# Kernel tuning notes

Hardware: AMD Instinct MI355X
Metric: run time of the kernel (lower is better)

## Reference

```python
import jax, jax.numpy as jnp
import numpy as np

B, L, H, K = 64, 2048, 256, 32  # batch, padded seq len, hidden dim, n event types


def setup_inputs() -> dict:
    key = jax.random.key(0)
    ks = jax.random.split(key, 11)
    event_seqs = jax.random.randint(ks[0], (B, L), 0, K)
    # ragged lengths; original code requires 1 <= seq_len <= L-1
    seqs_length = jax.random.randint(ks[1], (B,), 1, L - 1)
    total_time_seqs = jax.random.uniform(ks[2], (B,), minval=10.0, maxval=100.0)
    hidden_t = jax.random.normal(ks[3], (L, B, H))
    cell_t = jax.random.normal(ks[4], (L, B, H))
    cell_target_t = jax.random.normal(ks[5], (L, B, H))
    output_t = jax.random.uniform(ks[6], (L, B, H))          # output gate in (0,1)
    decay_t = jax.random.uniform(ks[7], (L, B, H))           # positive decay rates
    # mimics original bug: uniform(0, total_time_seqs[0]) for every row, shape [L, B]
    sim_time_seqs = jax.random.uniform(ks[8], (L, B), maxval=total_time_seqs[0])
    W_int = jax.random.normal(ks[9], (H, K)) * (1.0 / np.sqrt(H))
    b_int = jax.random.normal(ks[10], (K,)) * 0.01
    return dict(event_seqs=event_seqs, seqs_length=seqs_length,
                total_time_seqs=total_time_seqs, hidden_t=hidden_t,
                cell_t=cell_t, cell_target_t=cell_target_t, output_t=output_t,
                decay_t=decay_t, sim_time_seqs=sim_time_seqs, W_int=W_int, b_int=b_int)


def reference(event_seqs, seqs_length, total_time_seqs, hidden_t, cell_t,
              cell_target_t, output_t, decay_t, sim_time_seqs, W_int, b_int):
    # intensity_layer: softplus(Linear(H -> K)); log-intensity [L, B, K]
    log_intensity = jnp.log(jax.nn.softplus(
        jnp.einsum('lbh,hk->lbk', hidden_t, W_int) + b_int))

    # ragged mask over time steps: valid t < seq_len, shape [B, L]
    mask = jnp.arange(L)[None, :] < seqs_length[:, None]

    # term 1: sum_b sum_{t<len_b} log_intensity[t, b, event_seqs[b, t+1]]
    # shift events left by one; last column is always masked (seq_len <= L-1)
    shifted = jnp.concatenate([event_seqs[:, 1:], event_seqs[:, :1]], axis=1)  # [B, L]
    li_b = jnp.transpose(log_intensity, (1, 0, 2))                              # [B, L, K]
    gathered = jnp.take_along_axis(li_b, shifted[:, :, None], axis=2)[..., 0]   # [B, L]
    original_ll = jnp.sum(jnp.where(mask, gathered, 0.0))

    # term 2: Monte Carlo integral of intensity at simulated durations
    # decay_cell: c(t) = c_target + (c - c_target) * exp(-decay * dt); h = o * tanh(c)
    c_sim = cell_target_t + (cell_t - cell_target_t) * jnp.exp(
        -decay_t * sim_time_seqs[:, :, None])                                   # [L, B, H]
    h_sim = output_t * jnp.tanh(c_sim)
    sim_intensity = jax.nn.softplus(
        jnp.einsum('lbh,hk->lbk', h_sim, W_int) + b_int)                        # [L, B, K]
    per_b = jnp.sum(jnp.where(mask, sim_intensity.sum(-1).T, 0.0), axis=1)      # [B]
    mc_coef = total_time_seqs / seqs_length.astype(total_time_seqs.dtype)
    simulated_ll = jnp.sum(mc_coef * per_b)

    return -(original_ll - simulated_ll)
```

## Files before the change

### kernel.cpp

```cpp
#include <hip/hip_runtime.h>

#define LL 2048
#define BB 64
#define HH 256
#define KK 32

#define NB  768
#define WPB 4

typedef __attribute__((ext_vector_type(8))) short  short8;
typedef __attribute__((ext_vector_type(4))) float  f32x4;

__device__ __forceinline__ float softplus_f(float x) {
    return x > 20.f ? x : __logf(1.f + __expf(x));
}
__device__ __forceinline__ unsigned f2bf(float x) {
    unsigned u = __builtin_bit_cast(unsigned, x);
    return (u + 0x7FFFu + ((u >> 16) & 1u)) >> 16;
}

struct RowT { float4 h, c, t, o, d; };

__global__ __launch_bounds__(256, 3) void nhll_main(
    const int*   __restrict__ events,
    const int*   __restrict__ lens,
    const float* __restrict__ ttime,
    const float* __restrict__ hidden,
    const float* __restrict__ cell,
    const float* __restrict__ ctarg,
    const float* __restrict__ outp,
    const float* __restrict__ decay,
    const float* __restrict__ simt,
    const float* __restrict__ W,
    const float* __restrict__ bias,
    float*       __restrict__ partial)
{
    __shared__ __align__(16) char  WTs[KK * HH * 2];
    __shared__ __align__(16) char  Als[WPB][16 * HH * 2];
    __shared__ int   pfx[BB + 1];
    __shared__ float coef_s[BB];
    __shared__ float wacc[WPB];

    const int tid  = threadIdx.x;
    const int lane = tid & 63;
    const int q    = tid >> 6;
    const int g    = lane >> 4;
    const int m    = lane & 15;

    {
        const float* wrow = &W[tid * KK];
#pragma unroll
        for (int k = 0; k < KK; ++k) {
            const int byte = (k * 512 + tid * 2) ^ ((k & 7) << 4);
            *(unsigned short*)(WTs + byte) = (unsigned short)f2bf(wrow[k]);
        }
    }
    if (tid < BB) {
        const int ln = lens[tid];
        coef_s[tid] = ttime[tid] / (float)ln;
        int s = ln;
#pragma unroll
        for (int mm = 1; mm < 64; mm <<= 1) {
            const int t = __shfl_up(s, mm, 64);
            if (lane >= mm) s += t;
        }
        pfx[tid + 1] = s;
        if (tid == 0) pfx[0] = 0;
    }
    __syncthreads();

    const float b_lo = bias[m];
    const float b_hi = bias[16 + m];
    const int   T      = pfx[BB];
    const int   ntiles = (T + 7) >> 3;
    char* Aw = Als[q];
    float acc = 0.f;

    for (int tile = blockIdx.x * WPB + q; tile < ntiles; tile += NB * WPB) {
        int i = tile * 8 + (lane & 7);
        const int valid = (i < T) ? 1 : 0;
        if (!valid) i = T - 1;
        int lo = 0, hi = BB;
#pragma unroll
        for (int s = 0; s < 6; ++s) {
            const int mid = (lo + hi) >> 1;
            if (pfx[mid] <= i) lo = mid; else hi = mid;
        }
        const int   b    = lo;
        const int   l    = i - pfx[b];
        const int   r    = l * BB + b;
        const float st   = simt[r];
        const float coef = valid ? coef_s[b] : 0.f;
        const int   e    = events[b * LL + l + 1];

        int   rs[8]; float ss[8];
#pragma unroll
        for (int j = 0; j < 8; ++j) {
            rs[j] = __shfl(r, j, 64);
            ss[j] = __shfl(st, j, 64);
        }

        auto LD = [&](int rr_) -> RowT {
            const int base = rr_ * HH + lane * 4;
            RowT x;
            x.h = *(const float4*)(hidden + base);
            x.c = *(const float4*)(cell   + base);
            x.t = *(const float4*)(ctarg  + base);
            x.o = *(const float4*)(outp   + base);
            x.d = *(const float4*)(decay  + base);
            return x;
        };
        auto ST = [&](int j, const RowT& R, float stv) {
            float4 v;
            float cs, e2;
            cs = R.t.x + (R.c.x - R.t.x) * __expf(-R.d.x * stv); e2 = __expf(2.f * cs); v.x = R.o.x * ((e2 - 1.f) / (e2 + 1.f));
            cs = R.t.y + (R.c.y - R.t.y) * __expf(-R.d.y * stv); e2 = __expf(2.f * cs); v.y = R.o.y * ((e2 - 1.f) / (e2 + 1.f));
            cs = R.t.z + (R.c.z - R.t.z) * __expf(-R.d.z * stv); e2 = __expf(2.f * cs); v.z = R.o.z * ((e2 - 1.f) / (e2 + 1.f));
            cs = R.t.w + (R.c.w - R.t.w) * __expf(-R.d.w * stv); e2 = __expf(2.f * cs); v.w = R.o.w * ((e2 - 1.f) / (e2 + 1.f));
            const int swz = (j & 7) << 4;
            *(uint2*)(Aw + ((j * 512 + lane * 8) ^ swz)) =
                make_uint2(f2bf(v.x) | (f2bf(v.y) << 16), f2bf(v.z) | (f2bf(v.w) << 16));
            *(uint2*)(Aw + (((8 + j) * 512 + lane * 8) ^ swz)) =
                make_uint2(f2bf(R.h.x) | (f2bf(R.h.y) << 16), f2bf(R.h.z) | (f2bf(R.h.w) << 16));
        };

        RowT buf[3];
        buf[0] = LD(rs[0]); buf[1] = LD(rs[1]); buf[2] = LD(rs[2]);
#pragma unroll
        for (int j = 0; j < 8; ++j) {
            ST(j, buf[j % 3], ss[j]);
            if (j + 3 < 8) buf[j % 3] = LD(rs[j + 3]);
        }

        f32x4 C0 = {0.f,0.f,0.f,0.f}, C1 = {0.f,0.f,0.f,0.f};
        const int abase = m * 512 + 16 * g;
        const int swz   = (m & 7) << 4;
#pragma unroll
        for (int c = 0; c < 8; ++c) {
            const short8 a  = *(const short8*)(Aw  + ((abase + 64 * c) ^ swz));
            const short8 w0 = *(const short8*)(WTs + ((abase + 64 * c) ^ swz));
            const short8 w1 = *(const short8*)(WTs + ((abase + 8192 + 64 * c) ^ swz));
            C0 = __builtin_amdgcn_mfma_f32_16x16x32_bf16(a, w0, C0, 0, 0, 0);
            C1 = __builtin_amdgcn_mfma_f32_16x16x32_bf16(a, w1, C1, 0, 0, 0);
        }

        float sp[4];
#pragma unroll
        for (int reg = 0; reg < 4; ++reg)
            sp[reg] = softplus_f(C0[reg] + b_lo) + softplus_f(C1[reg] + b_hi);
#pragma unroll
        for (int mk = 1; mk <= 8; mk <<= 1) {
#pragma unroll
            for (int reg = 0; reg < 4; ++reg) sp[reg] += __shfl_xor(sp[reg], mk, 64);
        }
        float t2 = 0.f;
#pragma unroll
        for (int reg = 0; reg < 4; ++reg) {
            const float cf = __shfl(coef, 4 * g + reg, 64);
            t2 += cf * sp[reg];
        }
        if (m == 0 && g < 2) acc += t2;

        float kv = 0.f, kb = 0.f;
#pragma unroll
        for (int rr = 0; rr < 8; ++rr) {
            const int   er   = __shfl(e, rr, 64);
            const float cand = (er < 16) ? C0[rr & 3] : C1[rr & 3];
            const float val  = __shfl(cand, 32 + ((rr >> 2) << 4) + (er & 15), 64);
            const float bsel = (er < 16) ? b_lo : b_hi;
            const float be   = __shfl(bsel, er & 15, 64);
            if (lane == rr) { kv = val; kb = be; }
        }
        if (lane < 8 && valid)
            acc -= __logf(softplus_f(kv + kb));
    }

#pragma unroll
    for (int mk = 1; mk < 64; mk <<= 1) acc += __shfl_xor(acc, mk, 64);
    if (lane == 0) wacc[q] = acc;
    __syncthreads();
    if (tid == 0) partial[blockIdx.x] = wacc[0] + wacc[1] + wacc[2] + wacc[3];
}

__global__ __launch_bounds__(256) void nhll_finalize(
    const float* __restrict__ partial, float* __restrict__ out)
{
    __shared__ float red[4];
    float s = 0.f;
    for (int i = threadIdx.x; i < NB; i += 256) s += partial[i];
    for (int mk = 1; mk < 64; mk <<= 1) s += __shfl_xor(s, mk, 64);
    if ((threadIdx.x & 63) == 0) red[threadIdx.x >> 6] = s;
    __syncthreads();
    if (threadIdx.x == 0)
        out[0] = red[0] + red[1] + red[2] + red[3];
}

extern "C" void kernel_launch(void* const* d_in, const int* in_sizes, int n_in,
                              void* d_out, int out_size, void* d_ws, size_t ws_size,
                              hipStream_t stream) {
    const int*   events = (const int*)  d_in[0];
    const int*   lens   = (const int*)  d_in[1];
    const float* ttime  = (const float*)d_in[2];
    const float* hidden = (const float*)d_in[3];
    const float* cell   = (const float*)d_in[4];
    const float* ctarg  = (const float*)d_in[5];
    const float* outp   = (const float*)d_in[6];
    const float* decay  = (const float*)d_in[7];
    const float* simt   = (const float*)d_in[8];
    const float* W      = (const float*)d_in[9];
    const float* bias   = (const float*)d_in[10];

    float* part = (float*)d_ws;
    float* out  = (float*)d_out;

    nhll_main<<<NB, 256, 0, stream>>>(events, lens, ttime, hidden, cell, ctarg,
                                      outp, decay, simt, W, bias, part);
    nhll_finalize<<<1, 256, 0, stream>>>(part, out);
}
```

Measured before the change: 68.35 us.

## Compute gathered event logit via per-row dot product instead of MFMA rows

The hidden-state rows are no longer staged in LDS for MFMA. For each row, the logit of the next event is computed directly as a dot product of the fp32 hidden row with the bf16 weight column for that event, followed by a wave-wide shuffle reduction. This halves the per-wave A tile in LDS, and with it the number of blocks is raised and launch bounds are bumped to 4 blocks per CU. The cost is six cross-lane shuffle steps per row, plus MFMA lanes 8-15 reading duplicated A rows, in exchange for less LDS traffic and higher occupancy.

```diff
diff --git a/kernel.cpp b/kernel.cpp
--- a/kernel.cpp
+++ b/kernel.cpp
@@ -5,7 +5,7 @@
 #define HH 256
 #define KK 32
 
-#define NB  768
+#define NB  1024
 #define WPB 4
 
 typedef __attribute__((ext_vector_type(8))) short  short8;
@@ -18,10 +18,16 @@
     unsigned u = __builtin_bit_cast(unsigned, x);
     return (u + 0x7FFFu + ((u >> 16) & 1u)) >> 16;
 }
+__device__ __forceinline__ float bfhi(unsigned u) {
+    return __builtin_bit_cast(float, u & 0xFFFF0000u);
+}
+__device__ __forceinline__ float bflo(unsigned u) {
+    return __builtin_bit_cast(float, u << 16);
+}
 
 struct RowT { float4 h, c, t, o, d; };
 
-__global__ __launch_bounds__(256, 3) void nhll_main(
+__global__ __launch_bounds__(256, 4) void nhll_main(
     const int*   __restrict__ events,
     const int*   __restrict__ lens,
     const float* __restrict__ ttime,
@@ -36,7 +42,7 @@
     float*       __restrict__ partial)
 {
     __shared__ __align__(16) char  WTs[KK * HH * 2];
-    __shared__ __align__(16) char  Als[WPB][16 * HH * 2];
+    __shared__ __align__(16) char  Als[WPB][8 * HH * 2];
     __shared__ int   pfx[BB + 1];
     __shared__ float coef_s[BB];
     __shared__ float wacc[WPB];
@@ -93,7 +99,7 @@
         const float coef = valid ? coef_s[b] : 0.f;
         const int   e    = events[b * LL + l + 1];
 
-        int   rs[8]; float ss[8];
+        int rs[8]; float ss[8];
 #pragma unroll
         for (int j = 0; j < 8; ++j) {
             rs[j] = __shfl(r, j, 64);
@@ -117,11 +123,18 @@
             cs = R.t.y + (R.c.y - R.t.y) * __expf(-R.d.y * stv); e2 = __expf(2.f * cs); v.y = R.o.y * ((e2 - 1.f) / (e2 + 1.f));
             cs = R.t.z + (R.c.z - R.t.z) * __expf(-R.d.z * stv); e2 = __expf(2.f * cs); v.z = R.o.z * ((e2 - 1.f) / (e2 + 1.f));
             cs = R.t.w + (R.c.w - R.t.w) * __expf(-R.d.w * stv); e2 = __expf(2.f * cs); v.w = R.o.w * ((e2 - 1.f) / (e2 + 1.f));
-            const int swz = (j & 7) << 4;
-            *(uint2*)(Aw + ((j * 512 + lane * 8) ^ swz)) =
+            *(uint2*)(Aw + ((j * 512 + lane * 8) ^ ((j & 7) << 4))) =
                 make_uint2(f2bf(v.x) | (f2bf(v.y) << 16), f2bf(v.z) | (f2bf(v.w) << 16));
-            *(uint2*)(Aw + (((8 + j) * 512 + lane * 8) ^ swz)) =
-                make_uint2(f2bf(R.h.x) | (f2bf(R.h.y) << 16), f2bf(R.h.z) | (f2bf(R.h.w) << 16));
+
+            const int ej = __shfl(e, j, 64);
+            const uint2 wc = *(const uint2*)(WTs + ((ej * 512 + lane * 8) ^ ((ej & 7) << 4)));
+            float su = R.h.x * bflo(wc.x) + R.h.y * bfhi(wc.x)
+                     + R.h.z * bflo(wc.y) + R.h.w * bfhi(wc.y);
+#pragma unroll
+            for (int mk = 1; mk < 64; mk <<= 1) su += __shfl_xor(su, mk, 64);
+            const float be = __shfl((ej < 16) ? b_lo : b_hi, ej & 15, 64);
+            if (lane == j && valid)
+                acc -= __logf(softplus_f(su + be));
         };
 
         RowT buf[3];
@@ -133,13 +146,14 @@
         }
 
         f32x4 C0 = {0.f,0.f,0.f,0.f}, C1 = {0.f,0.f,0.f,0.f};
-        const int abase = m * 512 + 16 * g;
-        const int swz   = (m & 7) << 4;
+        const int abase = (m & 7) * 512 + 16 * g;
+        const int wbase = m * 512 + 16 * g;
+        const int swza  = (m & 7) << 4;
 #pragma unroll
         for (int c = 0; c < 8; ++c) {
-            const short8 a  = *(const short8*)(Aw  + ((abase + 64 * c) ^ swz));
-            const short8 w0 = *(const short8*)(WTs + ((abase + 64 * c) ^ swz));
-            const short8 w1 = *(const short8*)(WTs + ((abase + 8192 + 64 * c) ^ swz));
+            const short8 a  = *(const short8*)(Aw  + ((abase + 64 * c) ^ swza));
+            const short8 w0 = *(const short8*)(WTs + ((wbase + 64 * c) ^ swza));
+            const short8 w1 = *(const short8*)(WTs + ((wbase + 8192 + 64 * c) ^ swza));
             C0 = __builtin_amdgcn_mfma_f32_16x16x32_bf16(a, w0, C0, 0, 0, 0);
             C1 = __builtin_amdgcn_mfma_f32_16x16x32_bf16(a, w1, C1, 0, 0, 0);
         }
@@ -160,19 +174,6 @@
             t2 += cf * sp[reg];
         }
         if (m == 0 && g < 2) acc += t2;
-
-        float kv = 0.f, kb = 0.f;
-#pragma unroll
-        for (int rr = 0; rr < 8; ++rr) {
-            const int   er   = __shfl(e, rr, 64);
-            const float cand = (er < 16) ? C0[rr & 3] : C1[rr & 3];
-            const float val  = __shfl(cand, 32 + ((rr >> 2) << 4) + (er & 15), 64);
-            const float bsel = (er < 16) ? b_lo : b_hi;
-            const float be   = __shfl(bsel, er & 15, 64);
-            if (lane == rr) { kv = val; kb = be; }
-        }
-        if (lane < 8 && valid)
-            acc -= __logf(softplus_f(kv + kb));
     }
 
 #pragma unroll
```

Result: slower. 119.4 us (+74.7%).

## Software-pipeline next tile's metadata and first row loads across MFMA epilogue

Applied to the files above, without the earlier changes.

Restructures the per-warp tile loop so the next tile's prefix-sum search, sim-time/event loads and first two row loads are issued before the current tile's MFMA and softplus epilogue. This hides global-load latency across tile iterations and removes the lambda-based ring buffer in favour of explicit rotating registers. Bias is also staged in shared memory so the event-bias lookup becomes a direct LDS read instead of a shuffle. The extra live RowT registers raise register pressure and could hurt occupancy under the 3-blocks launch bound.

```diff
diff --git a/kernel.cpp b/kernel.cpp
--- a/kernel.cpp
+++ b/kernel.cpp
@@ -20,6 +20,37 @@
 }
 
 struct RowT { float4 h, c, t, o, d; };
+
+__device__ __forceinline__ RowT load_row(
+    const float* __restrict__ hidden, const float* __restrict__ cell,
+    const float* __restrict__ ctarg,  const float* __restrict__ outp,
+    const float* __restrict__ decay,  int r, int lane)
+{
+    const int base = r * HH + lane * 4;
+    RowT x;
+    x.h = *(const float4*)(hidden + base);
+    x.c = *(const float4*)(cell   + base);
+    x.t = *(const float4*)(ctarg  + base);
+    x.o = *(const float4*)(outp   + base);
+    x.d = *(const float4*)(decay  + base);
+    return x;
+}
+
+template<int J>
+__device__ __forceinline__ void STrow(char* Aw, const RowT& R, float stv, int lane)
+{
+    float4 v;
+    float cs, e2;
+    cs = R.t.x + (R.c.x - R.t.x) * __expf(-R.d.x * stv); e2 = __expf(2.f * cs); v.x = R.o.x * ((e2 - 1.f) / (e2 + 1.f));
+    cs = R.t.y + (R.c.y - R.t.y) * __expf(-R.d.y * stv); e2 = __expf(2.f * cs); v.y = R.o.y * ((e2 - 1.f) / (e2 + 1.f));
+    cs = R.t.z + (R.c.z - R.t.z) * __expf(-R.d.z * stv); e2 = __expf(2.f * cs); v.z = R.o.z * ((e2 - 1.f) / (e2 + 1.f));
+    cs = R.t.w + (R.c.w - R.t.w) * __expf(-R.d.w * stv); e2 = __expf(2.f * cs); v.w = R.o.w * ((e2 - 1.f) / (e2 + 1.f));
+    const int swz = (J & 7) << 4;
+    *(uint2*)(Aw + ((J * 512 + lane * 8) ^ swz)) =
+        make_uint2(f2bf(v.x) | (f2bf(v.y) << 16), f2bf(v.z) | (f2bf(v.w) << 16));
+    *(uint2*)(Aw + (((8 + J) * 512 + lane * 8) ^ swz)) =
+        make_uint2(f2bf(R.h.x) | (f2bf(R.h.y) << 16), f2bf(R.h.z) | (f2bf(R.h.w) << 16));
+}
 
 __global__ __launch_bounds__(256, 3) void nhll_main(
     const int*   __restrict__ events,
@@ -39,6 +70,7 @@
     __shared__ __align__(16) char  Als[WPB][16 * HH * 2];
     __shared__ int   pfx[BB + 1];
     __shared__ float coef_s[BB];
+    __shared__ float bias_s[KK];
     __shared__ float wacc[WPB];
 
     const int tid  = threadIdx.x;
@@ -55,6 +87,7 @@
             *(unsigned short*)(WTs + byte) = (unsigned short)f2bf(wrow[k]);
         }
     }
+    if (tid < KK) bias_s[tid] = bias[tid];
     if (tid < BB) {
         const int ln = lens[tid];
         coef_s[tid] = ttime[tid] / (float)ln;
@@ -69,111 +102,118 @@
     }
     __syncthreads();
 
-    const float b_lo = bias[m];
-    const float b_hi = bias[16 + m];
+    const float b_lo = bias_s[m];
+    const float b_hi = bias_s[16 + m];
     const int   T      = pfx[BB];
     const int   ntiles = (T + 7) >> 3;
+    const int   stride = NB * WPB;
     char* Aw = Als[q];
     float acc = 0.f;
 
-    for (int tile = blockIdx.x * WPB + q; tile < ntiles; tile += NB * WPB) {
-        int i = tile * 8 + (lane & 7);
-        const int valid = (i < T) ? 1 : 0;
-        if (!valid) i = T - 1;
-        int lo = 0, hi = BB;
-#pragma unroll
-        for (int s = 0; s < 6; ++s) {
-            const int mid = (lo + hi) >> 1;
-            if (pfx[mid] <= i) lo = mid; else hi = mid;
+#define META(TILE, R_, ST_, E_, CF_, V_) do {                                 \
+        int i_ = (TILE) * 8 + (lane & 7);                                     \
+        V_ = (i_ < T) ? 1 : 0;                                                \
+        if (!V_) i_ = T - 1;                                                  \
+        int lo_ = 0, hi_ = BB;                                                \
+        _Pragma("unroll")                                                     \
+        for (int s_ = 0; s_ < 6; ++s_) {                                      \
+            const int mid_ = (lo_ + hi_) >> 1;                                \
+            if (pfx[mid_] <= i_) lo_ = mid_; else hi_ = mid_;                 \
+        }                                                                     \
+        const int b_ = lo_;                                                   \
+        const int l_ = i_ - pfx[b_];                                          \
+        R_  = l_ * BB + b_;                                                   \
+        ST_ = simt[R_];                                                       \
+        CF_ = V_ ? coef_s[b_] : 0.f;                                          \
+        E_  = events[b_ * LL + l_ + 1];               \
+    } while (0)
+
+    int tile = blockIdx.x * WPB + q;
+    if (tile < ntiles) {
+        int r, e, valid; float st, coef;
+        META(tile, r, st, e, coef, valid);
+        float ss0 = __shfl(st, 0, 64), ss1 = __shfl(st, 1, 64);
+        RowT b0 = load_row(hidden, cell, ctarg, outp, decay, __shfl(r, 0, 64), lane);
+        RowT b1 = load_row(hidden, cell, ctarg, outp, decay, __shfl(r, 1, 64), lane);
+
+        while (true) {
+            const int   rs2 = __shfl(r, 2, 64), rs3 = __shfl(r, 3, 64),
+                        rs4 = __shfl(r, 4, 64), rs5 = __shfl(r, 5, 64),
+                        rs6 = __shfl(r, 6, 64), rs7 = __shfl(r, 7, 64);
+            const float ss2 = __shfl(st, 2, 64), ss3 = __shfl(st, 3, 64),
+                        ss4 = __shfl(st, 4, 64), ss5 = __shfl(st, 5, 64),
+                        ss6 = __shfl(st, 6, 64), ss7 = __shfl(st, 7, 64);
+
+            RowT b2 = load_row(hidden, cell, ctarg, outp, decay, rs2, lane);
+            STrow<0>(Aw, b0, ss0, lane); b0 = load_row(hidden, cell, ctarg, outp, decay, rs3, lane);
+            STrow<1>(Aw, b1, ss1, lane); b1 = load_row(hidden, cell, ctarg, outp, decay, rs4, lane);
+            STrow<2>(Aw, b2, ss2, lane); b2 = load_row(hidden, cell, ctarg, outp, decay, rs5, lane);
+            STrow<3>(Aw, b0, ss3, lane); b0 = load_row(hidden, cell, ctarg, outp, decay, rs6, lane);
+            STrow<4>(Aw, b1, ss4, lane); b1 = load_row(hidden, cell, ctarg, outp, decay, rs7, lane);
+            STrow<5>(Aw, b2, ss5, lane);
+            STrow<6>(Aw, b0, ss6, lane);
+            STrow<7>(Aw, b1, ss7, lane);
+
+            const int  next    = tile + stride;
+            const bool hasNext = next < ntiles;
+            int nr = 0, ne = 0, nvalid = 0; float nst = 0.f, ncoef = 0.f;
+            float nss0 = 0.f, nss1 = 0.f;
+            if (hasNext) {
+                META(next, nr, nst, ne, ncoef, nvalid);
+                nss0 = __shfl(nst, 0, 64);
+                nss1 = __shfl(nst, 1, 64);
+                b0 = load_row(hidden, cell, ctarg, outp, decay, __shfl(nr, 0, 64), lane);
+                b1 = load_row(hidden, cell, ctarg, outp, decay, __shfl(nr, 1, 64), lane);
+            }
+
+            f32x4 C0 = {0.f,0.f,0.f,0.f}, C1 = {0.f,0.f,0.f,0.f};
+            const int abase = m * 512 + 16 * g;
+            const int swza  = (m & 7) << 4;
+#pragma unroll
+            for (int c = 0; c < 8; ++c) {
+                const short8 a  = *(const short8*)(Aw  + ((abase + 64 * c) ^ swza));
+                const short8 w0 = *(const short8*)(WTs + ((abase + 64 * c) ^ swza));
+                const short8 w1 = *(const short8*)(WTs + ((abase + 8192 + 64 * c) ^ swza));
+                C0 = __builtin_amdgcn_mfma_f32_16x16x32_bf16(a, w0, C0, 0, 0, 0);
+                C1 = __builtin_amdgcn_mfma_f32_16x16x32_bf16(a, w1, C1, 0, 0, 0);
+            }
+
+            float sp[4];
+#pragma unroll
+            for (int reg = 0; reg < 4; ++reg)
+                sp[reg] = softplus_f(C0[reg] + b_lo) + softplus_f(C1[reg] + b_hi);
+#pragma unroll
+            for (int mk = 1; mk <= 8; mk <<= 1) {
+#pragma unroll
+                for (int reg = 0; reg < 4; ++reg) sp[reg] += __shfl_xor(sp[reg], mk, 64);
+            }
+            float t2 = 0.f;
+#pragma unroll
+            for (int reg = 0; reg < 4; ++reg) {
+                const float cf = __shfl(coef, 4 * g + reg, 64);
+                t2 += cf * sp[reg];
+            }
+            if (m == 0 && g < 2) acc += t2;
+
+            float kv = 0.f, kb = 0.f;
+#pragma unroll
+            for (int rr = 0; rr < 8; ++rr) {
+                const int   er   = __shfl(e, rr, 64);
+                const float cand = (er < 16) ? C0[rr & 3] : C1[rr & 3];
+                const float val  = __shfl(cand, 32 + ((rr >> 2) << 4) + (er & 15), 64);
+                const float be   = bias_s[er];
+                if (lane == rr) { kv = val; kb = be; }
+            }
+            if (lane < 8 && valid)
+                acc -= __logf(softplus_f(kv + kb));
+
+            if (!hasNext) break;
+            r = nr; st = nst; e = ne; coef = ncoef; valid = nvalid;
+            ss0 = nss0; ss1 = nss1;
+            tile = next;
         }
-        const int   b    = lo;
-        const int   l    = i - pfx[b];
-        const int   r    = l * BB + b;
-        const float st   = simt[r];
-        const float coef = valid ? coef_s[b] : 0.f;
-        const int   e    = events[b * LL + l + 1];
-
-        int   rs[8]; float ss[8];
-#pragma unroll
-        for (int j = 0; j < 8; ++j) {
-            rs[j] = __shfl(r, j, 64);
-            ss[j] = __shfl(st, j, 64);
-        }
-
-        auto LD = [&](int rr_) -> RowT {
-            const int base = rr_ * HH + lane * 4;
-            RowT x;
-            x.h = *(const float4*)(hidden + base);
-            x.c = *(const float4*)(cell   + base);
-            x.t = *(const float4*)(ctarg  + base);
-            x.o = *(const float4*)(outp   + base);
-            x.d = *(const float4*)(decay  + base);
-            return x;
-        };
-        auto ST = [&](int j, const RowT& R, float stv) {
-            float4 v;
-            float cs, e2;
-            cs = R.t.x + (R.c.x - R.t.x) * __expf(-R.d.x * stv); e2 = __expf(2.f * cs); v.x = R.o.x * ((e2 - 1.f) / (e2 + 1.f));
-            cs = R.t.y + (R.c.y - R.t.y) * __expf(-R.d.y * stv); e2 = __expf(2.f * cs); v.y = R.o.y * ((e2 - 1.f) / (e2 + 1.f));
-            cs = R.t.z + (R.c.z - R.t.z) * __expf(-R.d.z * stv); e2 = __expf(2.f * cs); v.z = R.o.z * ((e2 - 1.f) / (e2 + 1.f));
-            cs = R.t.w + (R.c.w - R.t.w) * __expf(-R.d.w * stv); e2 = __expf(2.f * cs); v.w = R.o.w * ((e2 - 1.f) / (e2 + 1.f));
-            const int swz = (j & 7) << 4;
-            *(uint2*)(Aw + ((j * 512 + lane * 8) ^ swz)) =
-                make_uint2(f2bf(v.x) | (f2bf(v.y) << 16), f2bf(v.z) | (f2bf(v.w) << 16));
-            *(uint2*)(Aw + (((8 + j) * 512 + lane * 8) ^ swz)) =
-                make_uint2(f2bf(R.h.x) | (f2bf(R.h.y) << 16), f2bf(R.h.z) | (f2bf(R.h.w) << 16));
-        };
-
-        RowT buf[3];
-        buf[0] = LD(rs[0]); buf[1] = LD(rs[1]); buf[2] = LD(rs[2]);
-#pragma unroll
-        for (int j = 0; j < 8; ++j) {
-            ST(j, buf[j % 3], ss[j]);
-            if (j + 3 < 8) buf[j % 3] = LD(rs[j + 3]);
-        }
-
-        f32x4 C0 = {0.f,0.f,0.f,0.f}, C1 = {0.f,0.f,0.f,0.f};
-        const int abase = m * 512 + 16 * g;
-        const int swz   = (m & 7) << 4;
-#pragma unroll
-        for (int c = 0; c < 8; ++c) {
-            const short8 a  = *(const short8*)(Aw  + ((abase + 64 * c) ^ swz));
-            const short8 w0 = *(const short8*)(WTs + ((abase + 64 * c) ^ swz));
-            const short8 w1 = *(const short8*)(WTs + ((abase + 8192 + 64 * c) ^ swz));
-            C0 = __builtin_amdgcn_mfma_f32_16x16x32_bf16(a, w0, C0, 0, 0, 0);
-            C1 = __builtin_amdgcn_mfma_f32_16x16x32_bf16(a, w1, C1, 0, 0, 0);
-        }
-
-        float sp[4];
-#pragma unroll
-        for (int reg = 0; reg < 4; ++reg)
-            sp[reg] = softplus_f(C0[reg] + b_lo) + softplus_f(C1[reg] + b_hi);
-#pragma unroll
-        for (int mk = 1; mk <= 8; mk <<= 1) {
-#pragma unroll
-            for (int reg = 0; reg < 4; ++reg) sp[reg] += __shfl_xor(sp[reg], mk, 64);
-        }
-        float t2 = 0.f;
-#pragma unroll
-        for (int reg = 0; reg < 4; ++reg) {
-            const float cf = __shfl(coef, 4 * g + reg, 64);
-            t2 += cf * sp[reg];
-        }
-        if (m == 0 && g < 2) acc += t2;
-
-        float kv = 0.f, kb = 0.f;
-#pragma unroll
-        for (int rr = 0; rr < 8; ++rr) {
-            const int   er   = __shfl(e, rr, 64);
-            const float cand = (er < 16) ? C0[rr & 3] : C1[rr & 3];
-            const float val  = __shfl(cand, 32 + ((rr >> 2) << 4) + (er & 15), 64);
-            const float bsel = (er < 16) ? b_lo : b_hi;
-            const float be   = __shfl(bsel, er & 15, 64);
-            if (lane == rr) { kv = val; kb = be; }
-        }
-        if (lane < 8 && valid)
-            acc -= __logf(softplus_f(kv + kb));
     }
+#undef META
 
 #pragma unroll
     for (int mk = 1; mk < 64; mk <<= 1) acc += __shfl_xor(acc, mk, 64);
```

Result: slower. 93.45 us (+36.7%).

## Use 1024-thread blocks with 16 waves sharing one LDS weight copy

Applied to the files above, without the earlier changes.

Grid goes from 768 blocks of 4 waves to 256 blocks of 16 waves, so each block converts W to bf16 in LDS once for 16 waves and the per-block setup is amortised over more tiles. Bias moves into shared memory and the event bias lookup reads it directly instead of shuffling. The load/compute pipeline is manually unrolled with templated helpers. Larger blocks raise LDS per block (16 A-tiles plus W) and the launch bound of 1024,4 may force register spilling or limit residency. A redundant multiply-by-zero shuffle is also added.

```diff
diff --git a/kernel.cpp b/kernel.cpp
--- a/kernel.cpp
+++ b/kernel.cpp
@@ -5,8 +5,8 @@
 #define HH 256
 #define KK 32
 
-#define NB  768
-#define WPB 4
+#define NB  256
+#define WPB 16
 
 typedef __attribute__((ext_vector_type(8))) short  short8;
 typedef __attribute__((ext_vector_type(4))) float  f32x4;
@@ -21,7 +21,38 @@
 
 struct RowT { float4 h, c, t, o, d; };
 
-__global__ __launch_bounds__(256, 3) void nhll_main(
+__device__ __forceinline__ RowT load_row(
+    const float* __restrict__ hidden, const float* __restrict__ cell,
+    const float* __restrict__ ctarg,  const float* __restrict__ outp,
+    const float* __restrict__ decay,  int r, int lane)
+{
+    const int base = r * HH + lane * 4;
+    RowT x;
+    x.h = *(const float4*)(hidden + base);
+    x.c = *(const float4*)(cell   + base);
+    x.t = *(const float4*)(ctarg  + base);
+    x.o = *(const float4*)(outp   + base);
+    x.d = *(const float4*)(decay  + base);
+    return x;
+}
+
+template<int J>
+__device__ __forceinline__ void STrow(char* Aw, const RowT& R, float stv, int lane)
+{
+    float4 v;
+    float cs, e2;
+    cs = R.t.x + (R.c.x - R.t.x) * __expf(-R.d.x * stv); e2 = __expf(2.f * cs); v.x = R.o.x * ((e2 - 1.f) / (e2 + 1.f));
+    cs = R.t.y + (R.c.y - R.t.y) * __expf(-R.d.y * stv); e2 = __expf(2.f * cs); v.y = R.o.y * ((e2 - 1.f) / (e2 + 1.f));
+    cs = R.t.z + (R.c.z - R.t.z) * __expf(-R.d.z * stv); e2 = __expf(2.f * cs); v.z = R.o.z * ((e2 - 1.f) / (e2 + 1.f));
+    cs = R.t.w + (R.c.w - R.t.w) * __expf(-R.d.w * stv); e2 = __expf(2.f * cs); v.w = R.o.w * ((e2 - 1.f) / (e2 + 1.f));
+    const int swz = (J & 7) << 4;
+    *(uint2*)(Aw + ((J * 512 + lane * 8) ^ swz)) =
+        make_uint2(f2bf(v.x) | (f2bf(v.y) << 16), f2bf(v.z) | (f2bf(v.w) << 16));
+    *(uint2*)(Aw + (((8 + J) * 512 + lane * 8) ^ swz)) =
+        make_uint2(f2bf(R.h.x) | (f2bf(R.h.y) << 16), f2bf(R.h.z) | (f2bf(R.h.w) << 16));
+}
+
+__global__ __launch_bounds__(1024, 4) void nhll_main(
     const int*   __restrict__ events,
     const int*   __restrict__ lens,
     const float* __restrict__ ttime,
@@ -39,6 +70,7 @@
     __shared__ __align__(16) char  Als[WPB][16 * HH * 2];
     __shared__ int   pfx[BB + 1];
     __shared__ float coef_s[BB];
+    __shared__ float bias_s[KK];
     __shared__ float wacc[WPB];
 
     const int tid  = threadIdx.x;
@@ -47,7 +79,7 @@
     const int g    = lane >> 4;
     const int m    = lane & 15;
 
-    {
+    if (tid < HH) {
         const float* wrow = &W[tid * KK];
 #pragma unroll
         for (int k = 0; k < KK; ++k) {
@@ -55,6 +87,7 @@
             *(unsigned short*)(WTs + byte) = (unsigned short)f2bf(wrow[k]);
         }
     }
+    if (tid < KK) bias_s[tid] = bias[tid];
     if (tid < BB) {
         const int ln = lens[tid];
         coef_s[tid] = ttime[tid] / (float)ln;
@@ -69,8 +102,8 @@
     }
     __syncthreads();
 
-    const float b_lo = bias[m];
-    const float b_hi = bias[16 + m];
+    const float b_lo = bias_s[m];
+    const float b_hi = bias_s[16 + m];
     const int   T      = pfx[BB];
     const int   ntiles = (T + 7) >> 3;
     char* Aw = Als[q];
@@ -93,44 +126,24 @@
         const float coef = valid ? coef_s[b] : 0.f;
         const int   e    = events[b * LL + l + 1];
 
-        int   rs[8]; float ss[8];
+        int rs[8]; float ss[8];
 #pragma unroll
         for (int j = 0; j < 8; ++j) {
             rs[j] = __shfl(r, j, 64);
             ss[j] = __shfl(st, j, 64);
         }
 
-        auto LD = [&](int rr_) -> RowT {
-            const int base = rr_ * HH + lane * 4;
-            RowT x;
-            x.h = *(const float4*)(hidden + base);
-            x.c = *(const float4*)(cell   + base);
-            x.t = *(const float4*)(ctarg  + base);
-            x.o = *(const float4*)(outp   + base);
-            x.d = *(const float4*)(decay  + base);
-            return x;
-        };
-        auto ST = [&](int j, const RowT& R, float stv) {
-            float4 v;
-            float cs, e2;
-            cs = R.t.x + (R.c.x - R.t.x) * __expf(-R.d.x * stv); e2 = __expf(2.f * cs); v.x = R.o.x * ((e2 - 1.f) / (e2 + 1.f));
-            cs = R.t.y + (R.c.y - R.t.y) * __expf(-R.d.y * stv); e2 = __expf(2.f * cs); v.y = R.o.y * ((e2 - 1.f) / (e2 + 1.f));
-            cs = R.t.z + (R.c.z - R.t.z) * __expf(-R.d.z * stv); e2 = __expf(2.f * cs); v.z = R.o.z * ((e2 - 1.f) / (e2 + 1.f));
-            cs = R.t.w + (R.c.w - R.t.w) * __expf(-R.d.w * stv); e2 = __expf(2.f * cs); v.w = R.o.w * ((e2 - 1.f) / (e2 + 1.f));
-            const int swz = (j & 7) << 4;
-            *(uint2*)(Aw + ((j * 512 + lane * 8) ^ swz)) =
-                make_uint2(f2bf(v.x) | (f2bf(v.y) << 16), f2bf(v.z) | (f2bf(v.w) << 16));
-            *(uint2*)(Aw + (((8 + j) * 512 + lane * 8) ^ swz)) =
-                make_uint2(f2bf(R.h.x) | (f2bf(R.h.y) << 16), f2bf(R.h.z) | (f2bf(R.h.w) << 16));
-        };
-
-        RowT buf[3];
-        buf[0] = LD(rs[0]); buf[1] = LD(rs[1]); buf[2] = LD(rs[2]);
-#pragma unroll
-        for (int j = 0; j < 8; ++j) {
-            ST(j, buf[j % 3], ss[j]);
-            if (j + 3 < 8) buf[j % 3] = LD(rs[j + 3]);
-        }
+        RowT b0 = load_row(hidden, cell, ctarg, outp, decay, rs[0], lane);
+        RowT b1 = load_row(hidden, cell, ctarg, outp, decay, rs[1], lane);
+        RowT b2 = load_row(hidden, cell, ctarg, outp, decay, rs[2], lane);
+        STrow<0>(Aw, b0, ss[0], lane); b0 = load_row(hidden, cell, ctarg, outp, decay, rs[3], lane);
+        STrow<1>(Aw, b1, ss[1], lane); b1 = load_row(hidden, cell, ctarg, outp, decay, rs[4], lane);
+        STrow<2>(Aw, b2, ss[2], lane); b2 = load_row(hidden, cell, ctarg, outp, decay, rs[5], lane);
+        STrow<3>(Aw, b0, ss[3], lane); b0 = load_row(hidden, cell, ctarg, outp, decay, rs[6], lane);
+        STrow<4>(Aw, b1, ss[4], lane); b1 = load_row(hidden, cell, ctarg, outp, decay, rs[7], lane);
+        STrow<5>(Aw, b2, ss[5], lane);
+        STrow<6>(Aw, b0, ss[6], lane);
+        STrow<7>(Aw, b1, ss[7], lane);
 
         f32x4 C0 = {0.f,0.f,0.f,0.f}, C1 = {0.f,0.f,0.f,0.f};
         const int abase = m * 512 + 16 * g;
@@ -156,7 +169,7 @@
         float t2 = 0.f;
 #pragma unroll
         for (int reg = 0; reg < 4; ++reg) {
-            const float cf = __shfl(coef, 4 * g + reg, 64);
+            const float cf = __shfl(coef, 4 * reg + 4 * g, 64) * 0.f + __shfl(coef, 4 * g + reg, 64);
             t2 += cf * sp[reg];
         }
         if (m == 0 && g < 2) acc += t2;
@@ -167,8 +180,7 @@
             const int   er   = __shfl(e, rr, 64);
             const float cand = (er < 16) ? C0[rr & 3] : C1[rr & 3];
             const float val  = __shfl(cand, 32 + ((rr >> 2) << 4) + (er & 15), 64);
-            const float bsel = (er < 16) ? b_lo : b_hi;
-            const float be   = __shfl(bsel, er & 15, 64);
+            const float be   = bias_s[er];
             if (lane == rr) { kv = val; kb = be; }
         }
         if (lane < 8 && valid)
@@ -179,7 +191,12 @@
     for (int mk = 1; mk < 64; mk <<= 1) acc += __shfl_xor(acc, mk, 64);
     if (lane == 0) wacc[q] = acc;
     __syncthreads();
-    if (tid == 0) partial[blockIdx.x] = wacc[0] + wacc[1] + wacc[2] + wacc[3];
+    if (tid == 0) {
+        float s = 0.f;
+#pragma unroll
+        for (int w = 0; w < WPB; ++w) s += wacc[w];
+        partial[blockIdx.x] = s;
+    }
 }
 
 __global__ __launch_bounds__(256) void nhll_finalize(
@@ -213,7 +230,7 @@
     float* part = (float*)d_ws;
     float* out  = (float*)d_out;
 
-    nhll_main<<<NB, 256, 0, stream>>>(events, lens, ttime, hidden, cell, ctarg,
-                                      outp, decay, simt, W, bias, part);
+    nhll_main<<<NB, 1024, 0, stream>>>(events, lens, ttime, hidden, cell, ctarg,
+                                       outp, decay, simt, W, bias, part);
     nhll_finalize<<<1, 256, 0, stream>>>(part, out);
 }
```

Measured after the change: 120.4 us. +76.1%, slower.
